# Performance work log

Hardware: AMD Instinct MI355X
Metric: run time of the kernel (lower is better)

The kernel has to match this reference:

```python
import jax, jax.numpy as jnp
import numpy as np

E = 8          # num experts
D = 1024       # hidden/model dim
H = 4096
B, S = 4, 2048


def setup_inputs() -> dict:
    key = jax.random.key(0)
    ks = jax.random.split(key, 4)
    x = jax.random.normal(ks[0], (B, S, D), dtype=jnp.float32)
    Wg = jax.random.normal(ks[1], (D, E), dtype=jnp.float32) * (1.0 / np.sqrt(D))
    W1 = jax.random.normal(ks[2], (E, D, H), dtype=jnp.float32) * (1.0 / np.sqrt(D))
    b1 = jnp.zeros((E, H), dtype=jnp.float32)
    W2 = jax.random.normal(ks[3], (E, H, D), dtype=jnp.float32) * (1.0 / np.sqrt(H))
    b2 = jnp.zeros((E, D), dtype=jnp.float32)
    return {"x": x, "Wg": Wg, "W1": W1, "b1": b1, "W2": W2, "b2": b2, "top_k": 2}


def reference(x, Wg, W1, b1, W2, b2, top_k):
    b, s, d = x.shape
    xt = x.reshape(-1, d)  # [T, D], T = total tokens
    # Linear gating: softmax over expert logits, select top_k, renormalize
    logits = xt @ Wg                                   # [T, E]
    probs = jax.nn.softmax(logits, axis=-1)            # [T, E]
    vals, idx = jax.lax.top_k(probs, top_k)            # [T, k]
    vals = vals / jnp.sum(vals, axis=-1, keepdims=True)
    # Combine weights: zero except at selected experts
    combine = jnp.sum(jax.nn.one_hot(idx, E, dtype=probs.dtype) * vals[..., None], axis=1)  # [T, E]
    # FFN experts (MLP with gelu), computed densely across experts
    h = jax.nn.gelu(jnp.einsum('td,edh->eth', xt, W1) + b1[:, None, :])  # [E, T, H]
    y = jnp.einsum('eth,ehd->etd', h, W2) + b2[:, None, :]               # [E, T, D]
    out = jnp.einsum('te,etd->td', combine, y)                           # [T, D]
    return out.reshape(b, s, d)
```

## Files before the change

kernel.cpp:

```cpp
#include <hip/hip_runtime.h>

#define T_TOK 8192
#define DIM   1024
#define HDIM  4096
#define NE    8
#define BK    64
#define BM    128
#define BN    128
#define SLOT_CAP (T_TOK * 2 + NE * BM)
#define TILES (SLOT_CAP / BM)

typedef float        f32x4 __attribute__((ext_vector_type(4)));
typedef unsigned int u32x4 __attribute__((ext_vector_type(4)));

__device__ inline unsigned short f2bf(float f) {
  union { float f; unsigned int u; } a; a.f = f;
  unsigned int u = a.u;
  unsigned int r = (u + 0x7FFFu + ((u >> 16) & 1u)) >> 16;
  return (unsigned short)r;
}

__device__ inline f32x4 mfma_bf16_16x16x32(u32x4 a, u32x4 b, f32x4 c) {
  asm("v_mfma_f32_16x16x32_bf16 %0, %1, %2, %0" : "+v"(c) : "v"(a), "v"(b));
  return c;
}

__device__ inline void gload_lds16(const void* g, void* l) {
  __builtin_amdgcn_global_load_lds(
      (const __attribute__((address_space(1))) void*)g,
      (__attribute__((address_space(3))) void*)l, 16, 0, 0);
}

__device__ inline float gelu_fast(float v) {
  const float c2 = 1.5957691216057308f;
  float z = c2 * (v + 0.044715f * v * v * v);
  return v / (1.0f + __expf(-z));
}

__device__ inline void load_offs(const int* __restrict__ counts, int* offs) {
  offs[0] = 0;
#pragma unroll
  for (int e = 0; e < NE; e++)
    offs[e + 1] = offs[e] + ((counts[e] + BM - 1) / BM) * BM;
}

__global__ __launch_bounds__(256) void transpose_bf16_kernel(const float* __restrict__ src,
                                                             unsigned short* __restrict__ dst,
                                                             int R, int C) {
  __shared__ float tile[64][65];
  int e  = blockIdx.z;
  int c0 = blockIdx.x * 64, r0 = blockIdx.y * 64;
  int c  = threadIdx.x & 63, r4 = threadIdx.x >> 6;
  const float* s = src + (size_t)e * R * C;
#pragma unroll
  for (int i = 0; i < 16; i++) {
    int r = r4 + i * 4;
    tile[r][c] = s[(size_t)(r0 + r) * C + (c0 + c)];
  }
  __syncthreads();
  unsigned short* d = dst + (size_t)e * R * C;
  int rbase = (threadIdx.x & 7) * 8;
#pragma unroll
  for (int g = 0; g < 2; g++) {
    int cc = (threadIdx.x >> 3) + g * 32;
    u32x4 v;
#pragma unroll
    for (int k = 0; k < 4; k++)
      v[k] = (unsigned int)f2bf(tile[rbase + 2 * k][cc])
           | ((unsigned int)f2bf(tile[rbase + 2 * k + 1][cc]) << 16);
    *(u32x4*)(d + (size_t)(c0 + cc) * R + (r0 + rbase)) = v;
  }
}

__global__ __launch_bounds__(256) void routing_kernel(const float* __restrict__ x,
                                                      const float* __restrict__ Wg,
                                                      int* __restrict__ tok_e,
                                                      float* __restrict__ tok_w,
                                                      unsigned short* __restrict__ xb,
                                                      int* __restrict__ counts) {
  __shared__ int h[NE];
  if (threadIdx.x < NE) h[threadIdx.x] = 0;
  __syncthreads();
  int tok  = (blockIdx.x * 256 + threadIdx.x) >> 6;
  int lane = threadIdx.x & 63;
  const float* xr = x + (size_t)tok * DIM;
  float acc[NE];
#pragma unroll
  for (int e = 0; e < NE; e++) acc[e] = 0.f;
  for (int d = lane; d < DIM; d += 64) {
    float xv = xr[d];
    const float* wr = Wg + d * NE;
#pragma unroll
    for (int e = 0; e < NE; e++) acc[e] += xv * wr[e];
  }
#pragma unroll
  for (int e = 0; e < NE; e++) {
#pragma unroll
    for (int off = 32; off > 0; off >>= 1) acc[e] += __shfl_xor(acc[e], off);
  }
  if (lane == 0) {
    int i0 = 0;
#pragma unroll
    for (int e = 1; e < NE; e++) if (acc[e] > acc[i0]) i0 = e;
    int i1 = (i0 == 0) ? 1 : 0;
#pragma unroll
    for (int e = 0; e < NE; e++) if (e != i0 && acc[e] > acc[i1]) i1 = e;
    float w0 = 1.0f / (1.0f + expf(acc[i1] - acc[i0]));
    tok_e[tok * 2]     = i0;
    tok_e[tok * 2 + 1] = i1;
    tok_w[tok * 2]     = w0;
    tok_w[tok * 2 + 1] = 1.0f - w0;
    atomicAdd(&h[i0], 1);
    atomicAdd(&h[i1], 1);
  }
  unsigned short* xo = xb + (size_t)tok * DIM;
#pragma unroll
  for (int i = 0; i < 4; i++) {
    f32x4 v = *(const f32x4*)(xr + lane * 16 + i * 4);
    unsigned long long p = (unsigned long long)f2bf(v[0])
                         | ((unsigned long long)f2bf(v[1]) << 16)
                         | ((unsigned long long)f2bf(v[2]) << 32)
                         | ((unsigned long long)f2bf(v[3]) << 48);
    *(unsigned long long*)(xo + lane * 16 + i * 4) = p;
  }
  __syncthreads();
  if (threadIdx.x < NE) atomicAdd(&counts[threadIdx.x], h[threadIdx.x]);
}

__global__ __launch_bounds__(256) void scatter_kernel(const int* __restrict__ tok_e,
                                                      const int* __restrict__ counts,
                                                      int* __restrict__ cursors,
                                                      int* __restrict__ slot_token,
                                                      int* __restrict__ tok_slot) {
  int offs[NE + 1];
  load_offs(counts, offs);
  int t = blockIdx.x * 256 + threadIdx.x;
  int lane = threadIdx.x & 63;
#pragma unroll
  for (int j = 0; j < 2; j++) {
    int e = tok_e[t * 2 + j];
#pragma unroll
    for (int ee = 0; ee < NE; ee++) {
      unsigned long long m = __ballot(e == ee);
      if (e == ee) {
        int leader = __ffsll(m) - 1;
        int base = 0;
        if (lane == leader) base = atomicAdd(&cursors[ee], (int)__popcll(m));
        base = __shfl(base, leader);
        int pos = base + (int)__popcll(m & ((1ULL << lane) - 1ULL));
        int s = offs[ee] + pos;
        slot_token[s] = t;
        tok_slot[t * 2 + j] = s;
      }
    }
  }
}


__global__ __launch_bounds__(256) void gemm1_kernel(const unsigned short* __restrict__ Xb,
                                                    const unsigned short* __restrict__ W1T,
                                                    const float* __restrict__ b1,
                                                    const int* __restrict__ slot_token,
                                                    const int* __restrict__ counts,
                                                    unsigned short* __restrict__ Hbuf) {
  __shared__ __align__(16) unsigned short As[BM][BK];
  __shared__ __align__(16) unsigned short Bs[BN][BK];
  int offs[NE + 1];
  load_offs(counts, offs);
  const int GY = HDIM / BN;
  int lin = blockIdx.y * gridDim.x + blockIdx.x;
  int cpx = (TILES * GY) >> 3;
  int wk  = (lin & 7) * cpx + (lin >> 3);
  int bx = wk / GY, by = wk % GY;

  int row0 = bx * BM;
  if (row0 >= offs[NE]) return;
  int e = 0;
#pragma unroll
  for (int i = 1; i < NE; i++) if (row0 >= offs[i]) e = i;
  int n0  = by * BN;
  int tid  = threadIdx.x;
  int lane = tid & 63;
  int w    = tid >> 6;
  int wr = tid >> 7;
  int wc = (tid >> 6) & 1;

  int lr  = lane >> 3;
  int lcx = (lane & 7) ^ lr;
  const unsigned short* aG[4];
  const unsigned short* bG[4];
  unsigned short* aL[4];
  unsigned short* bL[4];
#pragma unroll
  for (int i = 0; i < 4; i++) {
    int r = w * 32 + i * 8;
    int tk = slot_token[row0 + r + lr];
    if (tk < 0) tk = 0;
    aG[i] = Xb + (size_t)tk * DIM + lcx * 8;
    bG[i] = W1T + ((size_t)e * HDIM + n0 + r + lr) * DIM + lcx * 8;
    aL[i] = &As[r][0];
    bL[i] = &Bs[r][0];
  }

  int frow = lane & 15;
  int hi   = lane >> 4;
  int kxs  = (hi * 8) ^ ((lane & 7) << 3);

  f32x4 acc[4][4];
#pragma unroll
  for (int m = 0; m < 4; m++)
#pragma unroll
    for (int n = 0; n < 4; n++) acc[m][n] = 0.f;

  for (int k0 = 0; k0 < DIM; k0 += BK) {
#pragma unroll
    for (int i = 0; i < 4; i++) gload_lds16(aG[i] + k0, aL[i]);
#pragma unroll
    for (int i = 0; i < 4; i++) gload_lds16(bG[i] + k0, bL[i]);
    __syncthreads();
#pragma unroll
    for (int kk = 0; kk < 2; kk++) {
      int col = (kk * 32) ^ kxs;
      u32x4 a[4], b[4];
#pragma unroll
      for (int m = 0; m < 4; m++)
        a[m] = *(const u32x4*)&As[wr * 64 + m * 16 + frow][col];
#pragma unroll
      for (int n = 0; n < 4; n++)
        b[n] = *(const u32x4*)&Bs[wc * 64 + n * 16 + frow][col];
#pragma unroll
      for (int m = 0; m < 4; m++)
#pragma unroll
        for (int n = 0; n < 4; n++)
          acc[m][n] = mfma_bf16_16x16x32(a[m], b[n], acc[m][n]);
    }
    __syncthreads();
  }

  float bias[4];
#pragma unroll
  for (int n = 0; n < 4; n++) bias[n] = b1[e * HDIM + n0 + wc * 64 + n * 16 + frow];
  unsigned short (*E)[136] = (unsigned short (*)[136])(&As[0][0]);
#pragma unroll
  for (int c0 = 0; c0 < 128; c0 += 32) {
    if (wr == (c0 >> 6)) {
      int mbase = (c0 & 63) >> 4;
#pragma unroll
      for (int mm = 0; mm < 2; mm++) {
        int m = mbase + mm;
#pragma unroll
        for (int n = 0; n < 4; n++)
#pragma unroll
          for (int j = 0; j < 4; j++)
            E[mm * 16 + hi * 4 + j][wc * 64 + n * 16 + frow] =
                f2bf(gelu_fast(acc[m][n][j] + bias[n]));
      }
    }
    __syncthreads();
#pragma unroll
    for (int p = 0; p < 2; p++) {
      int r  = p * 16 + (tid >> 4);
      int cc = (tid & 15) * 8;
      u32x4 v = *(const u32x4*)&E[r][cc];
      *(u32x4*)(Hbuf + (size_t)(row0 + c0 + r) * HDIM + n0 + cc) = v;
    }
    __syncthreads();
  }
}

__global__ __launch_bounds__(256) void gemm2_kernel(const unsigned short* __restrict__ Hbuf,
                                                    const unsigned short* __restrict__ W2T,
                                                    const float* __restrict__ b2,
                                                    const int* __restrict__ counts,
                                                    unsigned short* __restrict__ Ybuf) {
  __shared__ __align__(16) unsigned short As[BM][BK];
  __shared__ __align__(16) unsigned short Bs[BN][BK];
  int offs[NE + 1];
  load_offs(counts, offs);
  const int GY = DIM / BN;
  int lin = blockIdx.y * gridDim.x + blockIdx.x;
  int cpx = (TILES * GY) >> 3;
  int wk  = (lin & 7) * cpx + (lin >> 3);
  int bx = wk / GY, by = wk % GY;

  int row0 = bx * BM;
  if (row0 >= offs[NE]) return;
  int e = 0;
#pragma unroll
  for (int i = 1; i < NE; i++) if (row0 >= offs[i]) e = i;
  int n0  = by * BN;
  int tid  = threadIdx.x;
  int lane = tid & 63;
  int w    = tid >> 6;
  int wr = tid >> 7;
  int wc = (tid >> 6) & 1;

  int lr  = lane >> 3;
  int lcx = (lane & 7) ^ lr;
  const unsigned short* aG[4];
  const unsigned short* bG[4];
  unsigned short* aL[4];
  unsigned short* bL[4];
#pragma unroll
  for (int i = 0; i < 4; i++) {
    int r = w * 32 + i * 8;
    aG[i] = Hbuf + (size_t)(row0 + r + lr) * HDIM + lcx * 8;
    bG[i] = W2T + ((size_t)e * DIM + n0 + r + lr) * HDIM + lcx * 8;
    aL[i] = &As[r][0];
    bL[i] = &Bs[r][0];
  }

  int frow = lane & 15;
  int hi   = lane >> 4;
  int kxs  = (hi * 8) ^ ((lane & 7) << 3);

  f32x4 acc[4][4];
#pragma unroll
  for (int m = 0; m < 4; m++)
#pragma unroll
    for (int n = 0; n < 4; n++) acc[m][n] = 0.f;

  for (int k0 = 0; k0 < HDIM; k0 += BK) {
#pragma unroll
    for (int i = 0; i < 4; i++) gload_lds16(aG[i] + k0, aL[i]);
#pragma unroll
    for (int i = 0; i < 4; i++) gload_lds16(bG[i] + k0, bL[i]);
    __syncthreads();
#pragma unroll
    for (int kk = 0; kk < 2; kk++) {
      int col = (kk * 32) ^ kxs;
      u32x4 a[4], b[4];
#pragma unroll
      for (int m = 0; m < 4; m++)
        a[m] = *(const u32x4*)&As[wr * 64 + m * 16 + frow][col];
#pragma unroll
      for (int n = 0; n < 4; n++)
        b[n] = *(const u32x4*)&Bs[wc * 64 + n * 16 + frow][col];
#pragma unroll
      for (int m = 0; m < 4; m++)
#pragma unroll
        for (int n = 0; n < 4; n++)
          acc[m][n] = mfma_bf16_16x16x32(a[m], b[n], acc[m][n]);
    }
    __syncthreads();
  }

  float bias[4];
#pragma unroll
  for (int n = 0; n < 4; n++) bias[n] = b2[e * DIM + n0 + wc * 64 + n * 16 + frow];
  unsigned short (*E)[136] = (unsigned short (*)[136])(&As[0][0]);
#pragma unroll
  for (int c0 = 0; c0 < 128; c0 += 32) {
    if (wr == (c0 >> 6)) {
      int mbase = (c0 & 63) >> 4;
#pragma unroll
      for (int mm = 0; mm < 2; mm++) {
        int m = mbase + mm;
#pragma unroll
        for (int n = 0; n < 4; n++)
#pragma unroll
          for (int j = 0; j < 4; j++)
            E[mm * 16 + hi * 4 + j][wc * 64 + n * 16 + frow] =
                f2bf(acc[m][n][j] + bias[n]);
      }
    }
    __syncthreads();
#pragma unroll
    for (int p = 0; p < 2; p++) {
      int r  = p * 16 + (tid >> 4);
      int cc = (tid & 15) * 8;
      u32x4 v = *(const u32x4*)&E[r][cc];
      *(u32x4*)(Ybuf + (size_t)(row0 + c0 + r) * DIM + n0 + cc) = v;
    }
    __syncthreads();
  }
}

__global__ __launch_bounds__(256) void combine_kernel(const unsigned short* __restrict__ Ybuf,
                                                      const int* __restrict__ tok_slot,
                                                      const float* __restrict__ tok_w,
                                                      float* __restrict__ out) {
  int t = blockIdx.x * 2 + (threadIdx.x >> 7);
  int c = (threadIdx.x & 127) * 8;
  int s0 = tok_slot[t * 2], s1 = tok_slot[t * 2 + 1];
  float w0 = tok_w[t * 2], w1 = tok_w[t * 2 + 1];
  u32x4 y0 = *(const u32x4*)(Ybuf + (size_t)s0 * DIM + c);
  u32x4 y1 = *(const u32x4*)(Ybuf + (size_t)s1 * DIM + c);
  float r[8];
#pragma unroll
  for (int k = 0; k < 4; k++) {
    union { unsigned int u; float f; } a0, b0, a1, b1;
    a0.u = y0[k] << 16; b0.u = y0[k] & 0xFFFF0000u;
    a1.u = y1[k] << 16; b1.u = y1[k] & 0xFFFF0000u;
    r[2 * k]     = w0 * a0.f + w1 * a1.f;
    r[2 * k + 1] = w0 * b0.f + w1 * b1.f;
  }
  float* o = out + (size_t)t * DIM + c;
  *(f32x4*)o       = *(f32x4*)&r[0];
  *(f32x4*)(o + 4) = *(f32x4*)&r[4];
}

extern "C" void kernel_launch(void* const* d_in, const int* in_sizes, int n_in,
                              void* d_out, int out_size, void* d_ws, size_t ws_size,
                              hipStream_t stream) {
  (void)in_sizes; (void)n_in; (void)out_size;
  const float* x  = (const float*)d_in[0];
  const float* Wg = (const float*)d_in[1];
  const float* W1 = (const float*)d_in[2];
  const float* b1 = (const float*)d_in[3];
  const float* W2 = (const float*)d_in[4];
  const float* b2 = (const float*)d_in[5];
  float* out = (float*)d_out;

  char* ws = (char*)d_ws;
  size_t off = 0;
  auto take = [&](size_t bytes) -> char* {
    char* p = ws + off;
    off += (bytes + 255) & ~(size_t)255;
    return p;
  };
  unsigned short* W1T  = (unsigned short*)take((size_t)NE * DIM * HDIM * 2);
  unsigned short* W2T  = (unsigned short*)take((size_t)NE * DIM * HDIM * 2);
  unsigned short* Xb   = (unsigned short*)take((size_t)T_TOK * DIM * 2);
  unsigned short* Hbuf = (unsigned short*)take((size_t)SLOT_CAP * HDIM * 2);
  unsigned short* Ybuf = (unsigned short*)take((size_t)SLOT_CAP * DIM * 2);
  int*   slot_token = (int*)take(SLOT_CAP * 4);
  int*   tok_e      = (int*)take(T_TOK * 2 * 4);
  float* tok_w      = (float*)take(T_TOK * 2 * 4);
  int*   tok_slot   = (int*)take(T_TOK * 2 * 4);
  int*   counts     = (int*)take(256);
  int*   cursors    = (int*)take(256);

  if (off > ws_size) {
    hipMemsetAsync(d_out, 0, (size_t)out_size * 4, stream);
    return;
  }

  hipMemsetAsync(counts, 0, 256, stream);
  hipMemsetAsync(cursors, 0, 256, stream);
  hipMemsetAsync(slot_token, 0xFF, SLOT_CAP * 4, stream);

  routing_kernel<<<T_TOK / 4, 256, 0, stream>>>(x, Wg, tok_e, tok_w, Xb, counts);
  scatter_kernel<<<T_TOK / 256, 256, 0, stream>>>(tok_e, counts, cursors, slot_token, tok_slot);
  transpose_bf16_kernel<<<dim3(HDIM / 64, DIM / 64, NE), 256, 0, stream>>>(W1, W1T, DIM, HDIM);
  transpose_bf16_kernel<<<dim3(DIM / 64, HDIM / 64, NE), 256, 0, stream>>>(W2, W2T, HDIM, DIM);
  gemm1_kernel<<<dim3(TILES, HDIM / BN), 256, 0, stream>>>(Xb, W1T, b1, slot_token, counts, Hbuf);
  gemm2_kernel<<<dim3(TILES, DIM / BN), 256, 0, stream>>>(Hbuf, W2T, b2, counts, Ybuf);
  combine_kernel<<<T_TOK / 2, 256, 0, stream>>>(Ybuf, tok_slot, tok_w, out);
}
```

Before: 531.3 us.

## Fuse routing and weight transposes, split-K gemm2, and trim memsets

Merges the routing kernel and both weight transposes into one prep launch, dispatching on block index. Replaces the full slot_token memset with padding-only fill inside the scatter kernel, and merges the two counter memsets into one. Splits gemm2 along K into two halves, doubling the grid to improve occupancy, with partial results written to a doubled Y buffer and summed in the combine kernel. This adds extra Y traffic and bf16 rounding of the partial sums.

```diff
diff --git a/kernel.cpp b/kernel.cpp
--- a/kernel.cpp
+++ b/kernel.cpp
@@ -44,12 +44,10 @@
     offs[e + 1] = offs[e] + ((counts[e] + BM - 1) / BM) * BM;
 }
 
-__global__ __launch_bounds__(256) void transpose_bf16_kernel(const float* __restrict__ src,
-                                                             unsigned short* __restrict__ dst,
-                                                             int R, int C) {
-  __shared__ float tile[64][65];
-  int e  = blockIdx.z;
-  int c0 = blockIdx.x * 64, r0 = blockIdx.y * 64;
+__device__ void transpose_body(const float* __restrict__ src,
+                               unsigned short* __restrict__ dst,
+                               int R, int C, int e, int c0, int r0,
+                               float (*tile)[65]) {
   int c  = threadIdx.x & 63, r4 = threadIdx.x >> 6;
   const float* s = src + (size_t)e * R * C;
 #pragma unroll
@@ -72,59 +70,75 @@
   }
 }
 
-__global__ __launch_bounds__(256) void routing_kernel(const float* __restrict__ x,
-                                                      const float* __restrict__ Wg,
-                                                      int* __restrict__ tok_e,
-                                                      float* __restrict__ tok_w,
-                                                      unsigned short* __restrict__ xb,
-                                                      int* __restrict__ counts) {
+__global__ __launch_bounds__(256) void prep_kernel(const float* __restrict__ x,
+                                                   const float* __restrict__ Wg,
+                                                   int* __restrict__ tok_e,
+                                                   float* __restrict__ tok_w,
+                                                   unsigned short* __restrict__ xb,
+                                                   int* __restrict__ counts,
+                                                   const float* __restrict__ W1,
+                                                   unsigned short* __restrict__ W1T,
+                                                   const float* __restrict__ W2,
+                                                   unsigned short* __restrict__ W2T) {
+  __shared__ float tile[64][65];
   __shared__ int h[NE];
-  if (threadIdx.x < NE) h[threadIdx.x] = 0;
-  __syncthreads();
-  int tok  = (blockIdx.x * 256 + threadIdx.x) >> 6;
-  int lane = threadIdx.x & 63;
-  const float* xr = x + (size_t)tok * DIM;
-  float acc[NE];
-#pragma unroll
-  for (int e = 0; e < NE; e++) acc[e] = 0.f;
-  for (int d = lane; d < DIM; d += 64) {
-    float xv = xr[d];
-    const float* wr = Wg + d * NE;
-#pragma unroll
-    for (int e = 0; e < NE; e++) acc[e] += xv * wr[e];
-  }
-#pragma unroll
-  for (int e = 0; e < NE; e++) {
-#pragma unroll
-    for (int off = 32; off > 0; off >>= 1) acc[e] += __shfl_xor(acc[e], off);
-  }
-  if (lane == 0) {
-    int i0 = 0;
-#pragma unroll
-    for (int e = 1; e < NE; e++) if (acc[e] > acc[i0]) i0 = e;
-    int i1 = (i0 == 0) ? 1 : 0;
-#pragma unroll
-    for (int e = 0; e < NE; e++) if (e != i0 && acc[e] > acc[i1]) i1 = e;
-    float w0 = 1.0f / (1.0f + expf(acc[i1] - acc[i0]));
-    tok_e[tok * 2]     = i0;
-    tok_e[tok * 2 + 1] = i1;
-    tok_w[tok * 2]     = w0;
-    tok_w[tok * 2 + 1] = 1.0f - w0;
-    atomicAdd(&h[i0], 1);
-    atomicAdd(&h[i1], 1);
-  }
-  unsigned short* xo = xb + (size_t)tok * DIM;
-#pragma unroll
-  for (int i = 0; i < 4; i++) {
-    f32x4 v = *(const f32x4*)(xr + lane * 16 + i * 4);
-    unsigned long long p = (unsigned long long)f2bf(v[0])
-                         | ((unsigned long long)f2bf(v[1]) << 16)
-                         | ((unsigned long long)f2bf(v[2]) << 32)
-                         | ((unsigned long long)f2bf(v[3]) << 48);
-    *(unsigned long long*)(xo + lane * 16 + i * 4) = p;
-  }
-  __syncthreads();
-  if (threadIdx.x < NE) atomicAdd(&counts[threadIdx.x], h[threadIdx.x]);
+  int bid = blockIdx.x;
+  if (bid < T_TOK / 4) {
+    if (threadIdx.x < NE) h[threadIdx.x] = 0;
+    __syncthreads();
+    int tok  = bid * 4 + (threadIdx.x >> 6);
+    int lane = threadIdx.x & 63;
+    const float* xr = x + (size_t)tok * DIM;
+    float acc[NE];
+#pragma unroll
+    for (int e = 0; e < NE; e++) acc[e] = 0.f;
+    for (int d = lane; d < DIM; d += 64) {
+      float xv = xr[d];
+      const float* wr = Wg + d * NE;
+#pragma unroll
+      for (int e = 0; e < NE; e++) acc[e] += xv * wr[e];
+    }
+#pragma unroll
+    for (int e = 0; e < NE; e++) {
+#pragma unroll
+      for (int off = 32; off > 0; off >>= 1) acc[e] += __shfl_xor(acc[e], off);
+    }
+    if (lane == 0) {
+      int i0 = 0;
+#pragma unroll
+      for (int e = 1; e < NE; e++) if (acc[e] > acc[i0]) i0 = e;
+      int i1 = (i0 == 0) ? 1 : 0;
+#pragma unroll
+      for (int e = 0; e < NE; e++) if (e != i0 && acc[e] > acc[i1]) i1 = e;
+      float w0 = 1.0f / (1.0f + expf(acc[i1] - acc[i0]));
+      tok_e[tok * 2]     = i0;
+      tok_e[tok * 2 + 1] = i1;
+      tok_w[tok * 2]     = w0;
+      tok_w[tok * 2 + 1] = 1.0f - w0;
+      atomicAdd(&h[i0], 1);
+      atomicAdd(&h[i1], 1);
+    }
+    unsigned short* xo = xb + (size_t)tok * DIM;
+#pragma unroll
+    for (int i = 0; i < 4; i++) {
+      f32x4 v = *(const f32x4*)(xr + lane * 16 + i * 4);
+      unsigned long long p = (unsigned long long)f2bf(v[0])
+                           | ((unsigned long long)f2bf(v[1]) << 16)
+                           | ((unsigned long long)f2bf(v[2]) << 32)
+                           | ((unsigned long long)f2bf(v[3]) << 48);
+      *(unsigned long long*)(xo + lane * 16 + i * 4) = p;
+    }
+    __syncthreads();
+    if (threadIdx.x < NE) atomicAdd(&counts[threadIdx.x], h[threadIdx.x]);
+  } else if (bid < T_TOK / 4 + 8192) {
+    int idx = bid - T_TOK / 4;
+    transpose_body(W1, W1T, DIM, HDIM, idx >> 10, (idx & 63) * 64,
+                   ((idx >> 6) & 15) * 64, tile);
+  } else {
+    int idx = bid - T_TOK / 4 - 8192;
+    transpose_body(W2, W2T, HDIM, DIM, idx >> 10, (idx & 15) * 64,
+                   ((idx >> 4) & 63) * 64, tile);
+  }
 }
 
 __global__ __launch_bounds__(256) void scatter_kernel(const int* __restrict__ tok_e,
@@ -134,6 +148,12 @@
                                                       int* __restrict__ tok_slot) {
   int offs[NE + 1];
   load_offs(counts, offs);
+  if (blockIdx.x == 0) {
+#pragma unroll
+    for (int e = 0; e < NE; e++)
+      for (int s = offs[e] + counts[e] + threadIdx.x; s < offs[e + 1]; s += 256)
+        slot_token[s] = -1;
+  }
   int t = blockIdx.x * 256 + threadIdx.x;
   int lane = threadIdx.x & 63;
 #pragma unroll
@@ -277,11 +297,14 @@
   __shared__ __align__(16) unsigned short Bs[BN][BK];
   int offs[NE + 1];
   load_offs(counts, offs);
-  const int GY = DIM / BN;
+  const int GY2 = (DIM / BN) * 2;
   int lin = blockIdx.y * gridDim.x + blockIdx.x;
-  int cpx = (TILES * GY) >> 3;
+  int cpx = (TILES * GY2) >> 3;
   int wk  = (lin & 7) * cpx + (lin >> 3);
-  int bx = wk / GY, by = wk % GY;
+  int bx = wk / GY2;
+  int rem = wk % GY2;
+  int by = rem & 7, sp = rem >> 3;
+  int kbase = sp * (HDIM / 2);
 
   int row0 = bx * BM;
   if (row0 >= offs[NE]) return;
@@ -304,8 +327,8 @@
 #pragma unroll
   for (int i = 0; i < 4; i++) {
     int r = w * 32 + i * 8;
-    aG[i] = Hbuf + (size_t)(row0 + r + lr) * HDIM + lcx * 8;
-    bG[i] = W2T + ((size_t)e * DIM + n0 + r + lr) * HDIM + lcx * 8;
+    aG[i] = Hbuf + (size_t)(row0 + r + lr) * HDIM + kbase + lcx * 8;
+    bG[i] = W2T + ((size_t)e * DIM + n0 + r + lr) * HDIM + kbase + lcx * 8;
     aL[i] = &As[r][0];
     bL[i] = &Bs[r][0];
   }
@@ -320,7 +343,7 @@
 #pragma unroll
     for (int n = 0; n < 4; n++) acc[m][n] = 0.f;
 
-  for (int k0 = 0; k0 < HDIM; k0 += BK) {
+  for (int k0 = 0; k0 < HDIM / 2; k0 += BK) {
 #pragma unroll
     for (int i = 0; i < 4; i++) gload_lds16(aG[i] + k0, aL[i]);
 #pragma unroll
@@ -347,7 +370,9 @@
 
   float bias[4];
 #pragma unroll
-  for (int n = 0; n < 4; n++) bias[n] = b2[e * DIM + n0 + wc * 64 + n * 16 + frow];
+  for (int n = 0; n < 4; n++)
+    bias[n] = sp ? b2[e * DIM + n0 + wc * 64 + n * 16 + frow] : 0.f;
+  unsigned short* Yp = Ybuf + (size_t)sp * SLOT_CAP * DIM;
   unsigned short (*E)[136] = (unsigned short (*)[136])(&As[0][0]);
 #pragma unroll
   for (int c0 = 0; c0 < 128; c0 += 32) {
@@ -370,7 +395,7 @@
       int r  = p * 16 + (tid >> 4);
       int cc = (tid & 15) * 8;
       u32x4 v = *(const u32x4*)&E[r][cc];
-      *(u32x4*)(Ybuf + (size_t)(row0 + c0 + r) * DIM + n0 + cc) = v;
+      *(u32x4*)(Yp + (size_t)(row0 + c0 + r) * DIM + n0 + cc) = v;
     }
     __syncthreads();
   }
@@ -384,16 +409,26 @@
   int c = (threadIdx.x & 127) * 8;
   int s0 = tok_slot[t * 2], s1 = tok_slot[t * 2 + 1];
   float w0 = tok_w[t * 2], w1 = tok_w[t * 2 + 1];
-  u32x4 y0 = *(const u32x4*)(Ybuf + (size_t)s0 * DIM + c);
-  u32x4 y1 = *(const u32x4*)(Ybuf + (size_t)s1 * DIM + c);
+  const unsigned short* Y1 = Ybuf + (size_t)SLOT_CAP * DIM;
+  u32x4 p0 = *(const u32x4*)(Ybuf + (size_t)s0 * DIM + c);
+  u32x4 p1 = *(const u32x4*)(Y1   + (size_t)s0 * DIM + c);
+  u32x4 q0 = *(const u32x4*)(Ybuf + (size_t)s1 * DIM + c);
+  u32x4 q1 = *(const u32x4*)(Y1   + (size_t)s1 * DIM + c);
   float r[8];
 #pragma unroll
   for (int k = 0; k < 4; k++) {
-    union { unsigned int u; float f; } a0, b0, a1, b1;
-    a0.u = y0[k] << 16; b0.u = y0[k] & 0xFFFF0000u;
-    a1.u = y1[k] << 16; b1.u = y1[k] & 0xFFFF0000u;
-    r[2 * k]     = w0 * a0.f + w1 * a1.f;
-    r[2 * k + 1] = w0 * b0.f + w1 * b1.f;
+    union { unsigned int u; float f; } a;
+#pragma unroll
+    for (int hl = 0; hl < 2; hl++) {
+      unsigned int sh = hl ? 0 : 16;
+      unsigned int msk = hl ? 0xFFFF0000u : 0xFFFFFFFFu;
+      a.u = hl ? (p0[k] & 0xFFFF0000u) : (p0[k] << 16); float vp0 = a.f;
+      a.u = hl ? (p1[k] & 0xFFFF0000u) : (p1[k] << 16); float vp1 = a.f;
+      a.u = hl ? (q0[k] & 0xFFFF0000u) : (q0[k] << 16); float vq0 = a.f;
+      a.u = hl ? (q1[k] & 0xFFFF0000u) : (q1[k] << 16); float vq1 = a.f;
+      (void)sh; (void)msk;
+      r[2 * k + hl] = w0 * (vp0 + vp1) + w1 * (vq0 + vq1);
+    }
   }
   float* o = out + (size_t)t * DIM + c;
   *(f32x4*)o       = *(f32x4*)&r[0];
@@ -423,28 +458,27 @@
   unsigned short* W2T  = (unsigned short*)take((size_t)NE * DIM * HDIM * 2);
   unsigned short* Xb   = (unsigned short*)take((size_t)T_TOK * DIM * 2);
   unsigned short* Hbuf = (unsigned short*)take((size_t)SLOT_CAP * HDIM * 2);
-  unsigned short* Ybuf = (unsigned short*)take((size_t)SLOT_CAP * DIM * 2);
+  unsigned short* Ybuf = (unsigned short*)take((size_t)2 * SLOT_CAP * DIM * 2);
   int*   slot_token = (int*)take(SLOT_CAP * 4);
   int*   tok_e      = (int*)take(T_TOK * 2 * 4);
   float* tok_w      = (float*)take(T_TOK * 2 * 4);
   int*   tok_slot   = (int*)take(T_TOK * 2 * 4);
-  int*   counts     = (int*)take(256);
-  int*   cursors    = (int*)take(256);
+  int*   cnt_cur    = (int*)take(256);
+  int*   counts  = cnt_cur;
+  int*   cursors = cnt_cur + 32;
 
   if (off > ws_size) {
     hipMemsetAsync(d_out, 0, (size_t)out_size * 4, stream);
     return;
   }
 
-  hipMemsetAsync(counts, 0, 256, stream);
-  hipMemsetAsync(cursors, 0, 256, stream);
-  hipMemsetAsync(slot_token, 0xFF, SLOT_CAP * 4, stream);
-
-  routing_kernel<<<T_TOK / 4, 256, 0, stream>>>(x, Wg, tok_e, tok_w, Xb, counts);
-  scatter_kernel<<<T_TOK / 256, 256, 0, stream>>>(tok_e, counts, cursors, slot_token, tok_slot);
-  transpose_bf16_kernel<<<dim3(HDIM / 64, DIM / 64, NE), 256, 0, stream>>>(W1, W1T, DIM, HDIM);
-  transpose_bf16_kernel<<<dim3(DIM / 64, HDIM / 64, NE), 256, 0, stream>>>(W2, W2T, HDIM, DIM);
-  gemm1_kernel<<<dim3(TILES, HDIM / BN), 256, 0, stream>>>(Xb, W1T, b1, slot_token, counts, Hbuf);
-  gemm2_kernel<<<dim3(TILES, DIM / BN), 256, 0, stream>>>(Hbuf, W2T, b2, counts, Ybuf);
+  hipMemsetAsync(cnt_cur, 0, 256, stream);
+  prep_kernel<<<T_TOK / 4 + 16384, 256, 0, stream>>>(x, Wg, tok_e, tok_w, Xb,
+                                                     counts, W1, W1T, W2, W2T);
+  scatter_kernel<<<T_TOK / 256, 256, 0, stream>>>(tok_e, counts, cursors,
+                                                  slot_token, tok_slot);
+  gemm1_kernel<<<dim3(TILES, HDIM / BN), 256, 0, stream>>>(Xb, W1T, b1,
+                                                           slot_token, counts, Hbuf);
+  gemm2_kernel<<<dim3(TILES, 16), 256, 0, stream>>>(Hbuf, W2T, b2, counts, Ybuf);
   combine_kernel<<<T_TOK / 2, 256, 0, stream>>>(Ybuf, tok_slot, tok_w, out);
 }
```

After: 497.8 us. -6.3%, faster.
